# Kernel tuning notes

Hardware: AMD Instinct MI355X
Metric: run time of the kernel (lower is better)

Reference implementation:

```python
import jax, jax.numpy as jnp
import numpy as np

EMB = 4096
HEADS = 32
SCALE = 4
D = EMB // HEADS          # qkv_dim = 128
HKV = HEADS // SCALE      # 8 kv heads
B, S = 2, 2048


def setup_inputs() -> dict:
    key = jax.random.key(0)
    ks = jax.random.split(key, 7)
    std = 0.02
    return {
        "x": jax.random.normal(ks[0], (B, S, EMB), jnp.float32),
        "Wq": jax.random.normal(ks[1], (EMB, D, HEADS), jnp.float32) * std,
        "bq": jnp.zeros((D, HEADS), jnp.float32),
        "Wk": jax.random.normal(ks[2], (EMB, D, HKV), jnp.float32) * std,
        "bk": jnp.zeros((D, HKV), jnp.float32),
        "Wv": jax.random.normal(ks[3], (EMB, D, HKV), jnp.float32) * std,
        "bv": jnp.zeros((D, HKV), jnp.float32),
    }


def reference(x, Wq, bq, Wk, bk, Wv, bv):
    # DenseGeneral projections: (B,S,E) -> (B,S,D,H)
    q = jnp.einsum("bse,edh->bsdh", x, Wq) + bq          # [B,S,D,H]
    k = jnp.einsum("bse,edh->bsdh", x, Wk) + bk          # [B,S,D,Hkv]
    v = jnp.einsum("bse,edh->bsdh", x, Wv) + bv          # [B,S,D,Hkv]
    # repeat kv heads (each kv head duplicated SCALE times, matching jnp.repeat)
    k = jnp.repeat(k, SCALE, axis=-1)                    # [B,S,D,H]
    v = jnp.repeat(v, SCALE, axis=-1)                    # [B,S,D,H]
    # NOTE: as written in the source, attention contracts the HEAD axis per
    # token: scores are (qkv_dim x qkv_dim) per (b, s) position.
    scores = jnp.einsum("bsdh,bseh->bsde", q, k) / np.float32(np.sqrt(D))
    attn = jax.nn.softmax(scores, axis=-1)               # [B,S,D,D]
    out = jnp.einsum("bsde,bseh->bsdh", attn, v)         # [B,S,D,H]
    return out.reshape(x.shape[:-1] + (EMB,))
```

## Files before the change

### kernel.cpp

```cpp
#include <hip/hip_runtime.h>
#include <cstdint>

typedef unsigned short ushort_t;
typedef __bf16 bf16x8 __attribute__((ext_vector_type(8)));
typedef float f32x4 __attribute__((ext_vector_type(4)));

__device__ __forceinline__ unsigned short f2bf(float f) {
  unsigned u = __builtin_bit_cast(unsigned, f);
  u += 0x7FFFu + ((u >> 16) & 1u);
  return (unsigned short)(u >> 16);
}
__device__ __forceinline__ float bflo(unsigned u) {
  return __builtin_bit_cast(float, u << 16);
}
__device__ __forceinline__ float bfhi(unsigned u) {
  return __builtin_bit_cast(float, u & 0xFFFF0000u);
}
__device__ __forceinline__ void gld16(const void* g, void* l) {
  auto* gp = reinterpret_cast<const __attribute__((address_space(1))) unsigned*>(
      reinterpret_cast<uintptr_t>(g));
  auto* lp = reinterpret_cast<__attribute__((address_space(3))) unsigned*>(
      reinterpret_cast<uintptr_t>(l));
  __builtin_amdgcn_global_load_lds(gp, lp, 16, 0, 0);
}

__global__ __launch_bounds__(256) void prep_all(
    const float* __restrict__ x, const float* __restrict__ Wq,
    const float* __restrict__ Wk, const float* __restrict__ Wv,
    const float* __restrict__ bq, const float* __restrict__ bk,
    const float* __restrict__ bv, ushort_t* __restrict__ Ax,
    ushort_t* __restrict__ Wt, float* __restrict__ bias) {
  __shared__ ushort_t red[64][65];
  const int b = blockIdx.x;
  const int tid = threadIdx.x;
  if (b < 3072) {
    const int ntile = b % 48, ktile = b / 48;
    const int n0 = ntile * 64, k0 = ktile * 64;
    if (ntile < 16) {
      for (int i = tid; i < 64 * 64; i += 256) {
        const int kk = i >> 6, nn = i & 63;
        const float4 w = *reinterpret_cast<const float4*>(
            Wq + (size_t)(k0 + kk) * 4096 + (size_t)(n0 + nn) * 4);
        red[kk][nn] = f2bf(w.x + w.y + w.z + w.w);
      }
    } else {
      const float* W = (ntile < 32) ? Wk : Wv;
      const int nb = (ntile < 32) ? (n0 - 1024) : (n0 - 2048);
      for (int i = tid; i < 64 * 64; i += 256) {
        const int kk = i >> 6, nn = i & 63;
        red[kk][nn] = f2bf(W[(size_t)(k0 + kk) * 1024 + nb + nn]);
      }
    }
    __syncthreads();
    for (int i = tid; i < 64 * 64; i += 256) {
      const int kk = i & 63, nn = i >> 6;
      Wt[(size_t)(n0 + nn) * 4096 + k0 + kk] = red[kk][nn];
    }
  } else if (b < 11264) {
    const size_t i = ((size_t)(b - 3072) * 256 + tid) * 8;
    const float4 a = *reinterpret_cast<const float4*>(x + i);
    const float4 c = *reinterpret_cast<const float4*>(x + i + 4);
    union { ushort_t u[8]; uint4 v; } pk;
    pk.u[0] = f2bf(a.x); pk.u[1] = f2bf(a.y); pk.u[2] = f2bf(a.z); pk.u[3] = f2bf(a.w);
    pk.u[4] = f2bf(c.x); pk.u[5] = f2bf(c.y); pk.u[6] = f2bf(c.z); pk.u[7] = f2bf(c.w);
    *reinterpret_cast<uint4*>(Ax + i) = pk.v;
  } else {
    const int n = (b - 11264) * 256 + tid;
    float v;
    if (n < 1024) {
      const float4 w = *reinterpret_cast<const float4*>(bq + (size_t)n * 4);
      v = w.x + w.y + w.z + w.w;
    } else if (n < 2048) {
      v = bk[n - 1024];
    } else {
      v = bv[n - 2048];
    }
    bias[n] = v;
  }
}

__global__ __launch_bounds__(256, 2) void gemm_qkv(const ushort_t* __restrict__ A,
                                                   const ushort_t* __restrict__ Bt,
                                                   const float* __restrict__ bias,
                                                   ushort_t* __restrict__ C) {
  __shared__ ushort_t As[128 * 64];
  __shared__ ushort_t Bs[128 * 64];
  const int tid = threadIdx.x;
  const int lane = tid & 63, wave = tid >> 6;
  const int M0 = blockIdx.y * 128, N0 = blockIdx.x * 128;

  const int rik = lane >> 3;
  const int gch = (lane & 7) ^ rik;
  const ushort_t* aG = A + (size_t)(M0 + wave * 32 + rik) * 4096 + gch * 8;
  const ushort_t* bG = Bt + (size_t)(N0 + wave * 32 + rik) * 4096 + gch * 8;

  const int wm = wave >> 1, wn = wave & 1;
  const int quad = lane >> 4, l15 = lane & 15;

  f32x4 acc[4][4];
  const f32x4 z = {0.f, 0.f, 0.f, 0.f};
#pragma unroll
  for (int mi = 0; mi < 4; ++mi)
#pragma unroll
    for (int ni = 0; ni < 4; ++ni) acc[mi][ni] = z;

  for (int kt = 0; kt < 64; ++kt) {
    const int ko = kt * 64;
#pragma unroll
    for (int q = 0; q < 4; ++q)
      gld16(aG + ko + q * (8 * 4096), &As[(wave * 4 + q) * 512]);
#pragma unroll
    for (int q = 0; q < 4; ++q)
      gld16(bG + ko + q * (8 * 4096), &Bs[(wave * 4 + q) * 512]);
    __syncthreads();
#pragma unroll
    for (int ks = 0; ks < 2; ++ks) {
      bf16x8 af[4], bfr[4];
#pragma unroll
      for (int mi = 0; mi < 4; ++mi) {
        const int row = wm * 64 + mi * 16 + l15;
        const int ch = ((ks * 4 + quad) ^ (row & 7)) * 8;
        af[mi] = *reinterpret_cast<const bf16x8*>(&As[row * 64 + ch]);
      }
#pragma unroll
      for (int ni = 0; ni < 4; ++ni) {
        const int row = wn * 64 + ni * 16 + l15;
        const int ch = ((ks * 4 + quad) ^ (row & 7)) * 8;
        bfr[ni] = *reinterpret_cast<const bf16x8*>(&Bs[row * 64 + ch]);
      }
#pragma unroll
      for (int mi = 0; mi < 4; ++mi)
#pragma unroll
        for (int ni = 0; ni < 4; ++ni)
          acc[mi][ni] =
              __builtin_amdgcn_mfma_f32_16x16x32_bf16(af[mi], bfr[ni], acc[mi][ni], 0, 0, 0);
    }
    __syncthreads();
  }

#pragma unroll
  for (int ni = 0; ni < 4; ++ni) {
    const int cc = N0 + wn * 64 + ni * 16 + l15;
    const float bn = bias[cc];
#pragma unroll
    for (int mi = 0; mi < 4; ++mi) {
      const int r0 = M0 + wm * 64 + mi * 16 + quad * 4;
#pragma unroll
      for (int r = 0; r < 4; ++r)
        C[(size_t)(r0 + r) * 3072 + cc] = f2bf(acc[mi][ni][r] + bn);
    }
  }
}

__global__ __launch_bounds__(256, 4) void attn_tok(const ushort_t* __restrict__ C,
                                                   float* __restrict__ out) {
  __shared__ uint4 kv4[4][256];
  const int tid = threadIdx.x;
  const int lane = tid & 63, wv = tid >> 6;
  const int t = blockIdx.x * 4 + wv;
  const ushort_t* Crow = C + (size_t)t * 3072;

  const uint4* src = reinterpret_cast<const uint4*>(Crow + 1024);
#pragma unroll
  for (int r = 0; r < 4; ++r) kv4[wv][r * 64 + lane] = src[r * 64 + lane];
  __syncthreads();

  const uint4 q01 = *reinterpret_cast<const uint4*>(Crow + lane * 16);
  const uint4 q23 = *reinterpret_cast<const uint4*>(Crow + lane * 16 + 8);
  float qa[8], qb[8];
  qa[0] = bflo(q01.x); qa[1] = bfhi(q01.x); qa[2] = bflo(q01.y); qa[3] = bfhi(q01.y);
  qa[4] = bflo(q01.z); qa[5] = bfhi(q01.z); qa[6] = bflo(q01.w); qa[7] = bfhi(q01.w);
  qb[0] = bflo(q23.x); qb[1] = bfhi(q23.x); qb[2] = bflo(q23.y); qb[3] = bfhi(q23.y);
  qb[4] = bflo(q23.z); qb[5] = bfhi(q23.z); qb[6] = bflo(q23.w); qb[7] = bfhi(q23.w);

  const uint4* kvw = kv4[wv];
  const float sc = 0.08838834764831845f;
  float oa[8], ob[8];
#pragma unroll
  for (int j = 0; j < 8; ++j) { oa[j] = 0.f; ob[j] = 0.f; }
  float l0 = 0.f, l1 = 0.f;

#pragma unroll 2
  for (int e = 0; e < 128; ++e) {
    const uint4 kr = kvw[e];
    float kf[8];
    kf[0] = bflo(kr.x); kf[1] = bfhi(kr.x); kf[2] = bflo(kr.y); kf[3] = bfhi(kr.y);
    kf[4] = bflo(kr.z); kf[5] = bfhi(kr.z); kf[6] = bflo(kr.w); kf[7] = bfhi(kr.w);
    float s0 = 0.f, s1 = 0.f;
#pragma unroll
    for (int j = 0; j < 8; ++j) { s0 += qa[j] * kf[j]; s1 += qb[j] * kf[j]; }
    const float p0 = __expf(s0 * sc);
    const float p1 = __expf(s1 * sc);
    l0 += p0; l1 += p1;
    const uint4 vr = kvw[128 + e];
    float vf[8];
    vf[0] = bflo(vr.x); vf[1] = bfhi(vr.x); vf[2] = bflo(vr.y); vf[3] = bfhi(vr.y);
    vf[4] = bflo(vr.z); vf[5] = bfhi(vr.z); vf[6] = bflo(vr.w); vf[7] = bfhi(vr.w);
#pragma unroll
    for (int j = 0; j < 8; ++j) { oa[j] += p0 * vf[j]; ob[j] += p1 * vf[j]; }
  }

  const float i0 = 1.f / l0, i1 = 1.f / l1;
  float4* dst = reinterpret_cast<float4*>(out + (size_t)t * 4096 + (size_t)lane * 64);
#pragma unroll
  for (int j = 0; j < 8; ++j) {
    const float w = oa[j] * i0;
    dst[j] = make_float4(w, w, w, w);
  }
#pragma unroll
  for (int j = 0; j < 8; ++j) {
    const float w = ob[j] * i1;
    dst[8 + j] = make_float4(w, w, w, w);
  }
}

extern "C" void kernel_launch(void* const* d_in, const int* in_sizes, int n_in,
                              void* d_out, int out_size, void* d_ws, size_t ws_size,
                              hipStream_t stream) {
  const float* x  = (const float*)d_in[0];
  const float* Wq = (const float*)d_in[1];
  const float* bq = (const float*)d_in[2];
  const float* Wk = (const float*)d_in[3];
  const float* bk = (const float*)d_in[4];
  const float* Wv = (const float*)d_in[5];
  const float* bv = (const float*)d_in[6];
  float* out = (float*)d_out;

  ushort_t* Ax = (ushort_t*)d_out;
  ushort_t* Wt = Ax + (size_t)4096 * 4096;
  float* bias = (float*)(Wt + (size_t)3072 * 4096);
  ushort_t* Cmat = (ushort_t*)d_ws;

  prep_all<<<dim3(11276), 256, 0, stream>>>(x, Wq, Wk, Wv, bq, bk, bv, Ax, Wt, bias);
  gemm_qkv<<<dim3(24, 32), 256, 0, stream>>>(Ax, Wt, bias, Cmat);
  attn_tok<<<dim3(1024), 256, 0, stream>>>(Cmat, out);
}
```

Before: 360.3 us.

## Double-buffer GEMM LDS tiles to overlap global loads with MFMA compute

The QKV GEMM now keeps two LDS buffers for the A and B tiles. It issues the async global-to-LDS loads for the next k-tile before computing on the current one, so load latency overlaps with MFMA work, and it uses a single waitcnt plus barrier per iteration. It also raises wave priority around the MFMA block with s_setprio. LDS use doubles to 64KB per block, which may cut occupancy below the two blocks per CU requested in launch bounds.

Result: no change. 357.6 us (-0.7%).

```diff
diff --git a/kernel.cpp b/kernel.cpp
--- a/kernel.cpp
+++ b/kernel.cpp
@@ -79,12 +79,20 @@
   }
 }
 
+#define WAITV0() asm volatile("s_waitcnt vmcnt(0)" ::: "memory")
+#define BARRIER()                         \
+  do {                                    \
+    __builtin_amdgcn_s_barrier();         \
+    asm volatile("" ::: "memory");        \
+    __builtin_amdgcn_sched_barrier(0);    \
+  } while (0)
+
 __global__ __launch_bounds__(256, 2) void gemm_qkv(const ushort_t* __restrict__ A,
                                                    const ushort_t* __restrict__ Bt,
                                                    const float* __restrict__ bias,
                                                    ushort_t* __restrict__ C) {
-  __shared__ ushort_t As[128 * 64];
-  __shared__ ushort_t Bs[128 * 64];
+  __shared__ ushort_t As[2][128 * 64];
+  __shared__ ushort_t Bs[2][128 * 64];
   const int tid = threadIdx.x;
   const int lane = tid & 63, wave = tid >> 6;
   const int M0 = blockIdx.y * 128, N0 = blockIdx.x * 128;
@@ -104,15 +112,23 @@
 #pragma unroll
     for (int ni = 0; ni < 4; ++ni) acc[mi][ni] = z;
 
+  auto stage = [&](int bb, int kt) {
+    const int ko = kt * 64;
+#pragma unroll
+    for (int q = 0; q < 4; ++q)
+      gld16(aG + ko + q * (8 * 4096), &As[bb][(wave * 4 + q) * 512]);
+#pragma unroll
+    for (int q = 0; q < 4; ++q)
+      gld16(bG + ko + q * (8 * 4096), &Bs[bb][(wave * 4 + q) * 512]);
+  };
+
+  stage(0, 0);
+  WAITV0();
+  BARRIER();
+
   for (int kt = 0; kt < 64; ++kt) {
-    const int ko = kt * 64;
-#pragma unroll
-    for (int q = 0; q < 4; ++q)
-      gld16(aG + ko + q * (8 * 4096), &As[(wave * 4 + q) * 512]);
-#pragma unroll
-    for (int q = 0; q < 4; ++q)
-      gld16(bG + ko + q * (8 * 4096), &Bs[(wave * 4 + q) * 512]);
-    __syncthreads();
+    const int bb = kt & 1;
+    if (kt < 63) stage(bb ^ 1, kt + 1);
 #pragma unroll
     for (int ks = 0; ks < 2; ++ks) {
       bf16x8 af[4], bfr[4];
@@ -120,22 +136,25 @@
       for (int mi = 0; mi < 4; ++mi) {
         const int row = wm * 64 + mi * 16 + l15;
         const int ch = ((ks * 4 + quad) ^ (row & 7)) * 8;
-        af[mi] = *reinterpret_cast<const bf16x8*>(&As[row * 64 + ch]);
+        af[mi] = *reinterpret_cast<const bf16x8*>(&As[bb][row * 64 + ch]);
       }
 #pragma unroll
       for (int ni = 0; ni < 4; ++ni) {
         const int row = wn * 64 + ni * 16 + l15;
         const int ch = ((ks * 4 + quad) ^ (row & 7)) * 8;
-        bfr[ni] = *reinterpret_cast<const bf16x8*>(&Bs[row * 64 + ch]);
-      }
+        bfr[ni] = *reinterpret_cast<const bf16x8*>(&Bs[bb][row * 64 + ch]);
+      }
+      __builtin_amdgcn_s_setprio(1);
 #pragma unroll
       for (int mi = 0; mi < 4; ++mi)
 #pragma unroll
         for (int ni = 0; ni < 4; ++ni)
           acc[mi][ni] =
               __builtin_amdgcn_mfma_f32_16x16x32_bf16(af[mi], bfr[ni], acc[mi][ni], 0, 0, 0);
-    }
-    __syncthreads();
+      __builtin_amdgcn_s_setprio(0);
+    }
+    WAITV0();
+    BARRIER();
   }
 
 #pragma unroll
```
